# Kernel optimization log

Measured on AMD Instinct MI355X. Metric: run time of the kernel, lower is better.

Reference implementation:

```python
import jax, jax.numpy as jnp
import numpy as np

B, C, H, W = 16, 512, 32, 32
G = min(C // 4, 32)  # group-norm groups = 32
EPS = 1e-6


def setup_inputs() -> dict:
    key = jax.random.key(0)
    ks = jax.random.split(key, 9)
    s = 1.0 / np.sqrt(C)
    return {
        "x": jax.random.normal(ks[0], (B, C, H, W), dtype=jnp.float32),
        "gn_gamma": jnp.ones((C,), jnp.float32),
        "gn_beta": jnp.zeros((C,), jnp.float32),
        "W0": jax.random.normal(ks[1], (C, C), jnp.float32) * s,
        "b0": jnp.zeros((C,), jnp.float32),
        "W1": jax.random.normal(ks[2], (C, C), jnp.float32) * s,
        "b1": jnp.zeros((C,), jnp.float32),
        "W2": jax.random.normal(ks[3], (C, C), jnp.float32) * s,
        "b2": jnp.zeros((C,), jnp.float32),
        "W3": jax.random.normal(ks[4], (C, C), jnp.float32) * s,
        "b3": jnp.zeros((C,), jnp.float32),
    }


def _group_norm(x, gamma, beta):
    b, c, h, w = x.shape
    xg = x.reshape(b, G, c // G, h, w)
    mu = jnp.mean(xg, axis=(2, 3, 4), keepdims=True)
    var = jnp.var(xg, axis=(2, 3, 4), keepdims=True)
    xn = ((xg - mu) * jax.lax.rsqrt(var + EPS)).reshape(b, c, h, w)
    return xn * gamma[None, :, None, None] + beta[None, :, None, None]


def _nin(x, Wm, bv):
    # 1x1 conv via channel contraction: bchw,cd->bdhw
    return jnp.einsum('bchw,cd->bdhw', x, Wm) + bv[None, :, None, None]


def reference(x, gn_gamma, gn_beta, W0, b0, W1, b1, W2, b2, W3, b3):
    b, c, h, w = x.shape
    hn = _group_norm(x, gn_gamma, gn_beta)
    q = _nin(hn, W0, b0)
    k = _nin(hn, W1, b1)
    v = _nin(hn, W2, b2)
    # attention scores over all spatial positions: [b, h, w, i, j]
    scores = jnp.einsum('bchw,bcij->bhwij', q, k) * (c ** -0.5)
    attn = jax.nn.softmax(scores.reshape(b, h, w, h * w), axis=-1).reshape(b, h, w, h, w)
    o = jnp.einsum('bhwij,bcij->bchw', attn, v)
    o = _nin(o, W3, b3)
    return x + o  # skip_rescale=False
```

## Files before the change

kernel.cpp:

```cpp
#include <hip/hip_runtime.h>
#include <stdint.h>

typedef __bf16 bf16_t;
typedef _Float16 f16_t;
typedef bf16_t bf16x8 __attribute__((ext_vector_type(8)));
typedef bf16_t bf16x4 __attribute__((ext_vector_type(4)));
typedef f16_t  f16x8  __attribute__((ext_vector_type(8)));
typedef f16_t  f16x4  __attribute__((ext_vector_type(4)));
typedef float floatx4 __attribute__((ext_vector_type(4)));

static constexpr int NB  = 16;
static constexpr int NC  = 512;
static constexpr int NHW = 1024;
static constexpr int NG  = 32;
static constexpr int CPG = 16;

#define SCALE 0.044194173824159216f
#define LOG2E 1.4426950408889634f

__global__ __launch_bounds__(256) void gn_stats_k(const float* __restrict__ x,
                                                  float* __restrict__ stats) {
  int bg = blockIdx.x;
  const float* xp = x + (size_t)bg * CPG * NHW;
  float s = 0.f, ss = 0.f;
  for (int i = threadIdx.x * 4; i < CPG * NHW; i += 256 * 4) {
    float4 v = *(const float4*)&xp[i];
    s += v.x + v.y + v.z + v.w;
    ss += v.x * v.x + v.y * v.y + v.z * v.z + v.w * v.w;
  }
#pragma unroll
  for (int off = 1; off < 64; off <<= 1) {
    s  += __shfl_xor(s,  off, 64);
    ss += __shfl_xor(ss, off, 64);
  }
  __shared__ float red[2][4];
  int wv = threadIdx.x >> 6;
  if ((threadIdx.x & 63) == 0) { red[0][wv] = s; red[1][wv] = ss; }
  __syncthreads();
  if (threadIdx.x == 0) {
    float st  = red[0][0] + red[0][1] + red[0][2] + red[0][3];
    float sst = red[1][0] + red[1][1] + red[1][2] + red[1][3];
    float mean = st * (1.f / 16384.f);
    float var  = sst * (1.f / 16384.f) - mean * mean;
    stats[bg * 2]     = mean;
    stats[bg * 2 + 1] = rsqrtf(var + 1e-6f);
  }
}

__global__ __launch_bounds__(256) void gn_apply_k(const float* __restrict__ x,
                                                  const float* __restrict__ gamma,
                                                  const float* __restrict__ beta,
                                                  const float* __restrict__ stats,
                                                  bf16_t* __restrict__ hnT) {
  int bi = blockIdx.z;
  int c0 = blockIdx.y * 32;
  int n0 = blockIdx.x * 32;
  __shared__ float tile[32][33];
  int tn = threadIdx.x & 31;
  int tr = threadIdx.x >> 5;
  const float* xb = x + (size_t)bi * NC * NHW;
#pragma unroll
  for (int r = 0; r < 4; r++) {
    int c = c0 + tr + r * 8;
    int g = c >> 4;
    float mean = stats[(bi * NG + g) * 2];
    float rstd = stats[(bi * NG + g) * 2 + 1];
    float ga = gamma[c], be = beta[c];
    float v = xb[(size_t)c * NHW + n0 + tn];
    tile[tr + r * 8][tn] = (v - mean) * rstd * ga + be;
  }
  __syncthreads();
  bf16_t* hb = hnT + (size_t)bi * NHW * NC;
  int nl = threadIdx.x >> 3, cc = (threadIdx.x & 7) * 4;
  bf16x4 pk;
#pragma unroll
  for (int i = 0; i < 4; i++) pk[i] = (bf16_t)tile[cc + i][nl];
  *(bf16x4*)&hb[(size_t)(n0 + nl) * NC + c0 + cc] = pk;
}

__global__ __launch_bounds__(256) void wtrans_k(const float* __restrict__ W0,
                                                const float* __restrict__ W1,
                                                const float* __restrict__ W2,
                                                const float* __restrict__ W3,
                                                bf16_t* __restrict__ Wt) {
  int w = blockIdx.z;
  const float* W = (w == 0) ? W0 : (w == 1) ? W1 : (w == 2) ? W2 : W3;
  int d0 = blockIdx.x * 32, c0 = blockIdx.y * 32;
  __shared__ float tile[32][33];
  int tdx = threadIdx.x & 31, tr = threadIdx.x >> 5;
#pragma unroll
  for (int r = 0; r < 4; r++)
    tile[tr + r * 8][tdx] = W[(size_t)(c0 + tr + r * 8) * NC + d0 + tdx];
  __syncthreads();
  bf16_t* o = Wt + (size_t)w * NC * NC;
  int dl = threadIdx.x >> 3, cc = (threadIdx.x & 7) * 4;
  bf16x4 pk;
#pragma unroll
  for (int i = 0; i < 4; i++) pk[i] = (bf16_t)tile[cc + i][dl];
  *(bf16x4*)&o[(size_t)(d0 + dl) * NC + c0 + cc] = pk;
}

__device__ __forceinline__ void glds16(const bf16_t* g, bf16_t* lds) {
  __builtin_amdgcn_global_load_lds(
      (const __attribute__((address_space(1))) unsigned int*)g,
      (__attribute__((address_space(3))) unsigned int*)lds, 16, 0, 0);
}

__device__ __forceinline__ floatx4 mfma_bf16(bf16x8 a, bf16x8 b, floatx4 c) {
  return __builtin_amdgcn_mfma_f32_16x16x32_bf16(a, b, c, 0, 0, 0);
}

template<int KDIM, bool SWAP>
__device__ __forceinline__ void gemm_core(const bf16_t* __restrict__ A,
                                          const bf16_t* __restrict__ B,
                                          int m0, int n0,
                                          floatx4 (&acc)[4][4]) {
  __shared__ bf16_t As[128 * 64];
  __shared__ bf16_t Bs[128 * 64];
  const int tid = threadIdx.x, lane = tid & 63, wv = tid >> 6;
  const int l16 = lane & 15, quad = lane >> 4;
  const int wm = wv & 1, wn = wv >> 1;
  const int x7 = l16 & 7;

  const int srow = lane >> 3;
  const int schunk = (lane & 7) ^ srow;
  const bf16_t* aptr = A + (size_t)(m0 + wv * 32 + srow) * KDIM + schunk * 8;
  const bf16_t* bptr = B + (size_t)(n0 + wv * 32 + srow) * KDIM + schunk * 8;
  bf16_t* as_ = &As[(wv * 32) * 64];
  bf16_t* bs_ = &Bs[(wv * 32) * 64];

  for (int k0 = 0; k0 < KDIM; k0 += 64) {
    __syncthreads();
#pragma unroll
    for (int i = 0; i < 4; i++) {
      glds16(aptr + (size_t)(8 * i) * KDIM, as_ + (8 * i) * 64);
      glds16(bptr + (size_t)(8 * i) * KDIM, bs_ + (8 * i) * 64);
    }
    aptr += 64; bptr += 64;
    __syncthreads();
    bf16x8 af[2][4], bfv[2][4];
#pragma unroll
    for (int h = 0; h < 2; h++)
#pragma unroll
      for (int i = 0; i < 4; i++) {
        int q = h * 4 + quad;
        af[h][i]  = *(const bf16x8*)&As[(wm * 64 + i * 16 + l16) * 64 + ((q ^ x7) * 8)];
        bfv[h][i] = *(const bf16x8*)&Bs[(wn * 64 + i * 16 + l16) * 64 + ((q ^ x7) * 8)];
      }
#pragma unroll
    for (int h = 0; h < 2; h++)
#pragma unroll
      for (int i = 0; i < 4; i++)
#pragma unroll
        for (int j = 0; j < 4; j++)
          acc[i][j] = SWAP ? mfma_bf16(bfv[h][j], af[h][i], acc[i][j])
                           : mfma_bf16(af[h][i], bfv[h][j], acc[i][j]);
  }
}

#define ACC_INIT(acc)                                   \
  floatx4 acc[4][4];                                    \
  _Pragma("unroll") for (int i = 0; i < 4; i++)         \
  _Pragma("unroll") for (int j = 0; j < 4; j++)         \
    acc[i][j] = (floatx4){0.f, 0.f, 0.f, 0.f};

__global__ __launch_bounds__(256) void gemm_qk_k(const bf16_t* __restrict__ hnT,
                                                 const bf16_t* __restrict__ Wt,
                                                 const float* __restrict__ b0,
                                                 const float* __restrict__ b1,
                                                 bf16_t* __restrict__ Qt,
                                                 bf16_t* __restrict__ Kt) {
  int bz = blockIdx.z, bi = bz & 15, wsel = bz >> 4;
  int n0 = blockIdx.x * 128, m0 = blockIdx.y * 128;
  const bf16_t* A = hnT + (size_t)bi * NHW * NC;
  const bf16_t* B = Wt + (size_t)wsel * NC * NC;
  ACC_INIT(acc);
  gemm_core<NC, true>(A, B, m0, n0, acc);

  const int lane = threadIdx.x & 63, wv = threadIdx.x >> 6;
  const int l16 = lane & 15, quad = lane >> 4, wm = wv & 1, wn = wv >> 1;
  const float* bias = wsel ? b1 : b0;
  bf16_t* out = (wsel ? Kt : Qt) + (size_t)bi * NHW * NC;
#pragma unroll
  for (int i = 0; i < 4; i++) {
    int m = m0 + wm * 64 + i * 16 + l16;
#pragma unroll
    for (int j = 0; j < 4; j++) {
      int db = n0 + wn * 64 + j * 16 + quad * 4;
      float4 bv = *(const float4*)&bias[db];
      bf16x4 pk;
      pk[0] = (bf16_t)(acc[i][j][0] + bv.x);
      pk[1] = (bf16_t)(acc[i][j][1] + bv.y);
      pk[2] = (bf16_t)(acc[i][j][2] + bv.z);
      pk[3] = (bf16_t)(acc[i][j][3] + bv.w);
      *(bf16x4*)&out[(size_t)m * NC + db] = pk;
    }
  }
}

__global__ __launch_bounds__(256) void gemm_v_k(const bf16_t* __restrict__ hnT,
                                                const bf16_t* __restrict__ Wt2,
                                                const float* __restrict__ b2,
                                                bf16_t* __restrict__ Vm) {
  int bi = blockIdx.z;
  int n0 = blockIdx.x * 128, m0 = blockIdx.y * 128;
  const bf16_t* A = hnT + (size_t)bi * NHW * NC;
  ACC_INIT(acc);
  gemm_core<NC, false>(A, Wt2, m0, n0, acc);

  const int lane = threadIdx.x & 63, wv = threadIdx.x >> 6;
  const int l16 = lane & 15, quad = lane >> 4, wm = wv & 1, wn = wv >> 1;
  bf16_t* out = Vm + (size_t)bi * NC * NHW;
#pragma unroll
  for (int i = 0; i < 4; i++)
#pragma unroll
    for (int j = 0; j < 4; j++) {
      int row = m0 + wm * 64 + i * 16 + quad * 4;
      int col = n0 + wn * 64 + j * 16 + l16;
      float bv = b2[col];
      bf16x4 pk;
#pragma unroll
      for (int r = 0; r < 4; r++) pk[r] = (bf16_t)(acc[i][j][r] + bv);
      *(bf16x4*)&out[(size_t)col * NHW + row] = pk;
    }
}

__global__ __launch_bounds__(256) void gemm_s_k(const bf16_t* __restrict__ Qt,
                                                const bf16_t* __restrict__ Kt,
                                                f16_t* __restrict__ S) {
  int bi = blockIdx.z;
  int n0 = blockIdx.x * 128, m0 = blockIdx.y * 128;
  const bf16_t* A = Qt + (size_t)bi * NHW * NC;
  const bf16_t* B = Kt + (size_t)bi * NHW * NC;
  ACC_INIT(acc);
  gemm_core<NC, true>(A, B, m0, n0, acc);

  const int lane = threadIdx.x & 63, wv = threadIdx.x >> 6;
  const int l16 = lane & 15, quad = lane >> 4, wm = wv & 1, wn = wv >> 1;
  f16_t* out = S + (size_t)bi * NHW * NHW;
#pragma unroll
  for (int i = 0; i < 4; i++) {
    int m = m0 + wm * 64 + i * 16 + l16;
#pragma unroll
    for (int j = 0; j < 4; j++) {
      int nb = n0 + wn * 64 + j * 16 + quad * 4;
      f16x4 pk;
#pragma unroll
      for (int r = 0; r < 4; r++) pk[r] = (f16_t)(acc[i][j][r] * SCALE);
      *(f16x4*)&out[(size_t)m * NHW + nb] = pk;
    }
  }
}

__global__ __launch_bounds__(256) void softmax_k(const f16_t* __restrict__ S,
                                                 bf16_t* __restrict__ P) {
  int row = blockIdx.x * 4 + (threadIdx.x >> 6);
  int lane = threadIdx.x & 63;
  const f16_t* sp = S + (size_t)row * NHW + lane * 16;
  f16x8 a = *(const f16x8*)sp;
  f16x8 b = *(const f16x8*)(sp + 8);
  float v[16];
#pragma unroll
  for (int k = 0; k < 8; k++) { v[k] = (float)a[k]; v[8 + k] = (float)b[k]; }
  float mx = v[0];
#pragma unroll
  for (int k = 1; k < 16; k++) mx = fmaxf(mx, v[k]);
#pragma unroll
  for (int off = 1; off < 64; off <<= 1) mx = fmaxf(mx, __shfl_xor(mx, off, 64));
  float e[16], s = 0.f;
#pragma unroll
  for (int k = 0; k < 16; k++) { e[k] = exp2f((v[k] - mx) * LOG2E); s += e[k]; }
#pragma unroll
  for (int off = 1; off < 64; off <<= 1) s += __shfl_xor(s, off, 64);
  float inv = 1.f / s;
  bf16x8 o0, o1;
#pragma unroll
  for (int k = 0; k < 8; k++) { o0[k] = (bf16_t)(e[k] * inv); o1[k] = (bf16_t)(e[8 + k] * inv); }
  bf16_t* pp = P + (size_t)row * NHW + lane * 16;
  *(bf16x8*)pp = o0;
  *(bf16x8*)(pp + 8) = o1;
}

__global__ __launch_bounds__(256) void gemm_pv_k(const bf16_t* __restrict__ P,
                                                 const bf16_t* __restrict__ Vm,
                                                 bf16_t* __restrict__ Ot) {
  int bi = blockIdx.z;
  int n0 = blockIdx.x * 128, m0 = blockIdx.y * 128;
  const bf16_t* A = P + (size_t)bi * NHW * NHW;
  const bf16_t* B = Vm + (size_t)bi * NC * NHW;
  ACC_INIT(acc);
  gemm_core<NHW, true>(A, B, m0, n0, acc);

  const int lane = threadIdx.x & 63, wv = threadIdx.x >> 6;
  const int l16 = lane & 15, quad = lane >> 4, wm = wv & 1, wn = wv >> 1;
  bf16_t* out = Ot + (size_t)bi * NHW * NC;
#pragma unroll
  for (int i = 0; i < 4; i++) {
    int m = m0 + wm * 64 + i * 16 + l16;
#pragma unroll
    for (int j = 0; j < 4; j++) {
      int cb = n0 + wn * 64 + j * 16 + quad * 4;
      bf16x4 pk;
#pragma unroll
      for (int r = 0; r < 4; r++) pk[r] = (bf16_t)(acc[i][j][r]);
      *(bf16x4*)&out[(size_t)m * NC + cb] = pk;
    }
  }
}

__global__ __launch_bounds__(256) void gemm_fin_k(const bf16_t* __restrict__ Ot,
                                                  const bf16_t* __restrict__ W3t,
                                                  const float* __restrict__ b3,
                                                  const float* __restrict__ x,
                                                  float* __restrict__ outp) {
  int bi = blockIdx.z;
  int n0 = blockIdx.x * 128, m0 = blockIdx.y * 128;
  const bf16_t* A = Ot + (size_t)bi * NHW * NC;
  ACC_INIT(acc);
  gemm_core<NC, false>(A, W3t, m0, n0, acc);

  const int lane = threadIdx.x & 63, wv = threadIdx.x >> 6;
  const int l16 = lane & 15, quad = lane >> 4, wm = wv & 1, wn = wv >> 1;
  const float* xb = x + (size_t)bi * NC * NHW;
  float* ob = outp + (size_t)bi * NC * NHW;
#pragma unroll
  for (int i = 0; i < 4; i++)
#pragma unroll
    for (int j = 0; j < 4; j++) {
      int row = m0 + wm * 64 + i * 16 + quad * 4;
      int col = n0 + wn * 64 + j * 16 + l16;
      float bv = b3[col];
      size_t base = (size_t)col * NHW + row;
      float4 xv = *(const float4*)&xb[base];
      float4 pk;
      pk.x = acc[i][j][0] + bv + xv.x;
      pk.y = acc[i][j][1] + bv + xv.y;
      pk.z = acc[i][j][2] + bv + xv.z;
      pk.w = acc[i][j][3] + bv + xv.w;
      *(float4*)&ob[base] = pk;
    }
}

extern "C" void kernel_launch(void* const* d_in, const int* in_sizes, int n_in,
                              void* d_out, int out_size, void* d_ws, size_t ws_size,
                              hipStream_t stream) {
  (void)in_sizes; (void)n_in; (void)out_size; (void)ws_size;
  const float* x     = (const float*)d_in[0];
  const float* gamma = (const float*)d_in[1];
  const float* beta  = (const float*)d_in[2];
  const float* W0    = (const float*)d_in[3];
  const float* b0    = (const float*)d_in[4];
  const float* W1    = (const float*)d_in[5];
  const float* b1    = (const float*)d_in[6];
  const float* W2    = (const float*)d_in[7];
  const float* b2    = (const float*)d_in[8];
  const float* W3    = (const float*)d_in[9];
  const float* b3    = (const float*)d_in[10];
  float* outp = (float*)d_out;

  char* ws = (char*)d_ws;
  const size_t PLANE = (size_t)NB * NHW * NC * sizeof(bf16_t);
  float* stats = (float*)ws;
  size_t off = 4096;
  bf16_t* hnT = (bf16_t*)(ws + off); off += PLANE;
  bf16_t* Qt  = (bf16_t*)(ws + off); off += PLANE;
  bf16_t* Kt  = (bf16_t*)(ws + off); off += PLANE;
  bf16_t* Vm  = (bf16_t*)(ws + off); off += PLANE;
  bf16_t* Wt  = (bf16_t*)(ws + off); off += 4 * (size_t)NC * NC * sizeof(bf16_t);
  f16_t*  S   = (f16_t*)(ws + off);  off += (size_t)NB * NHW * NHW * sizeof(f16_t);
  bf16_t* P   = (bf16_t*)S;
  bf16_t* Ot  = hnT;

  gn_stats_k<<<NB * NG, 256, 0, stream>>>(x, stats);
  gn_apply_k<<<dim3(32, 16, NB), 256, 0, stream>>>(x, gamma, beta, stats, hnT);
  wtrans_k<<<dim3(16, 16, 4), 256, 0, stream>>>(W0, W1, W2, W3, Wt);
  gemm_qk_k<<<dim3(4, 8, 32), 256, 0, stream>>>(hnT, Wt, b0, b1, Qt, Kt);
  gemm_v_k<<<dim3(4, 8, NB), 256, 0, stream>>>(hnT, Wt + 2 * (size_t)NC * NC, b2, Vm);
  gemm_s_k<<<dim3(8, 8, NB), 256, 0, stream>>>(Qt, Kt, S);
  softmax_k<<<dim3(NB * NHW / 4), 256, 0, stream>>>(S, P);
  gemm_pv_k<<<dim3(4, 8, NB), 256, 0, stream>>>(P, Vm, Ot);
  gemm_fin_k<<<dim3(4, 8, NB), 256, 0, stream>>>(Ot, Wt + 3 * (size_t)NC * NC, b3, x, outp);
}
```

Measured before the change: 257.9 us.

## Fold V projection into output projection via precomputed W2·W3 product

Removes the per-batch V projection GEMM by using the associativity attn·(hn·W2)·W3 = (attn·hn)·(W2·W3): a small kernel computes the combined 512x512 weight once and a bias kernel folds b2·W3+b3, since softmax rows sum to one. GroupNorm apply now also writes a channel-major copy of hn to serve as the PV operand. The softmax scale moves from the score GEMM epilogue into the Q projection epilogue. This trades one large GEMM for a tiny weight GEMM, a serial bias loop and an extra hn write, and adds bf16 rounding of the combined weight.

```diff
diff --git a/kernel.cpp b/kernel.cpp
--- a/kernel.cpp
+++ b/kernel.cpp
@@ -51,7 +51,8 @@
                                                   const float* __restrict__ gamma,
                                                   const float* __restrict__ beta,
                                                   const float* __restrict__ stats,
-                                                  bf16_t* __restrict__ hnT) {
+                                                  bf16_t* __restrict__ hnT,
+                                                  bf16_t* __restrict__ hnN) {
   int bi = blockIdx.z;
   int c0 = blockIdx.y * 32;
   int n0 = blockIdx.x * 32;
@@ -70,12 +71,17 @@
     tile[tr + r * 8][tn] = (v - mean) * rstd * ga + be;
   }
   __syncthreads();
+  int rl = threadIdx.x >> 3, ch = (threadIdx.x & 7) * 4;
   bf16_t* hb = hnT + (size_t)bi * NHW * NC;
-  int nl = threadIdx.x >> 3, cc = (threadIdx.x & 7) * 4;
   bf16x4 pk;
 #pragma unroll
-  for (int i = 0; i < 4; i++) pk[i] = (bf16_t)tile[cc + i][nl];
-  *(bf16x4*)&hb[(size_t)(n0 + nl) * NC + c0 + cc] = pk;
+  for (int i = 0; i < 4; i++) pk[i] = (bf16_t)tile[ch + i][rl];
+  *(bf16x4*)&hb[(size_t)(n0 + rl) * NC + c0 + ch] = pk;
+  bf16_t* hc = hnN + (size_t)bi * NC * NHW;
+  bf16x4 pk2;
+#pragma unroll
+  for (int i = 0; i < 4; i++) pk2[i] = (bf16_t)tile[rl][ch + i];
+  *(bf16x4*)&hc[(size_t)(c0 + rl) * NHW + n0 + ch] = pk2;
 }
 
 __global__ __launch_bounds__(256) void wtrans_k(const float* __restrict__ W0,
@@ -85,19 +91,37 @@
                                                 bf16_t* __restrict__ Wt) {
   int w = blockIdx.z;
   const float* W = (w == 0) ? W0 : (w == 1) ? W1 : (w == 2) ? W2 : W3;
+  bf16_t* o = Wt + (size_t)w * NC * NC;
   int d0 = blockIdx.x * 32, c0 = blockIdx.y * 32;
+  if (w == 2) {
+    int cl = threadIdx.x >> 3, dc = (threadIdx.x & 7) * 4;
+    float4 v = *(const float4*)&W[(size_t)(c0 + cl) * NC + d0 + dc];
+    bf16x4 pk;
+    pk[0] = (bf16_t)v.x; pk[1] = (bf16_t)v.y; pk[2] = (bf16_t)v.z; pk[3] = (bf16_t)v.w;
+    *(bf16x4*)&o[(size_t)(c0 + cl) * NC + d0 + dc] = pk;
+    return;
+  }
   __shared__ float tile[32][33];
   int tdx = threadIdx.x & 31, tr = threadIdx.x >> 5;
 #pragma unroll
   for (int r = 0; r < 4; r++)
     tile[tr + r * 8][tdx] = W[(size_t)(c0 + tr + r * 8) * NC + d0 + tdx];
   __syncthreads();
-  bf16_t* o = Wt + (size_t)w * NC * NC;
   int dl = threadIdx.x >> 3, cc = (threadIdx.x & 7) * 4;
   bf16x4 pk;
 #pragma unroll
   for (int i = 0; i < 4; i++) pk[i] = (bf16_t)tile[cc + i][dl];
   *(bf16x4*)&o[(size_t)(d0 + dl) * NC + c0 + cc] = pk;
+}
+
+__global__ __launch_bounds__(256) void bias_k(const float* __restrict__ b2,
+                                              const float* __restrict__ W3,
+                                              const float* __restrict__ b3,
+                                              float* __restrict__ bb) {
+  int e = blockIdx.x * 256 + threadIdx.x;
+  float s = b3[e];
+  for (int d = 0; d < NC; d++) s += b2[d] * W3[(size_t)d * NC + e];
+  bb[e] = s;
 }
 
 __device__ __forceinline__ void glds16(const bf16_t* g, bf16_t* lds) {
@@ -163,6 +187,26 @@
   _Pragma("unroll") for (int i = 0; i < 4; i++)         \
   _Pragma("unroll") for (int j = 0; j < 4; j++)         \
     acc[i][j] = (floatx4){0.f, 0.f, 0.f, 0.f};
+
+__global__ __launch_bounds__(256) void w23_k(const bf16_t* __restrict__ Wt3,
+                                             const bf16_t* __restrict__ W2b,
+                                             bf16_t* __restrict__ W23t) {
+  int n0 = blockIdx.x * 128, m0 = blockIdx.y * 128;
+  ACC_INIT(acc);
+  gemm_core<NC, false>(Wt3, W2b, m0, n0, acc);
+  const int lane = threadIdx.x & 63, wv = threadIdx.x >> 6;
+  const int l16 = lane & 15, quad = lane >> 4, wm = wv & 1, wn = wv >> 1;
+#pragma unroll
+  for (int i = 0; i < 4; i++)
+#pragma unroll
+    for (int j = 0; j < 4; j++) {
+      int row = m0 + wm * 64 + i * 16 + quad * 4;
+      int col = n0 + wn * 64 + j * 16 + l16;
+#pragma unroll
+      for (int r = 0; r < 4; r++)
+        W23t[(size_t)(row + r) * NC + col] = (bf16_t)acc[i][j][r];
+    }
+}
 
 __global__ __launch_bounds__(256) void gemm_qk_k(const bf16_t* __restrict__ hnT,
                                                  const bf16_t* __restrict__ Wt,
@@ -180,6 +224,7 @@
   const int lane = threadIdx.x & 63, wv = threadIdx.x >> 6;
   const int l16 = lane & 15, quad = lane >> 4, wm = wv & 1, wn = wv >> 1;
   const float* bias = wsel ? b1 : b0;
+  const float sc = wsel ? 1.f : SCALE;
   bf16_t* out = (wsel ? Kt : Qt) + (size_t)bi * NHW * NC;
 #pragma unroll
   for (int i = 0; i < 4; i++) {
@@ -189,40 +234,13 @@
       int db = n0 + wn * 64 + j * 16 + quad * 4;
       float4 bv = *(const float4*)&bias[db];
       bf16x4 pk;
-      pk[0] = (bf16_t)(acc[i][j][0] + bv.x);
-      pk[1] = (bf16_t)(acc[i][j][1] + bv.y);
-      pk[2] = (bf16_t)(acc[i][j][2] + bv.z);
-      pk[3] = (bf16_t)(acc[i][j][3] + bv.w);
+      pk[0] = (bf16_t)((acc[i][j][0] + bv.x) * sc);
+      pk[1] = (bf16_t)((acc[i][j][1] + bv.y) * sc);
+      pk[2] = (bf16_t)((acc[i][j][2] + bv.z) * sc);
+      pk[3] = (bf16_t)((acc[i][j][3] + bv.w) * sc);
       *(bf16x4*)&out[(size_t)m * NC + db] = pk;
     }
   }
-}
-
-__global__ __launch_bounds__(256) void gemm_v_k(const bf16_t* __restrict__ hnT,
-                                                const bf16_t* __restrict__ Wt2,
-                                                const float* __restrict__ b2,
-                                                bf16_t* __restrict__ Vm) {
-  int bi = blockIdx.z;
-  int n0 = blockIdx.x * 128, m0 = blockIdx.y * 128;
-  const bf16_t* A = hnT + (size_t)bi * NHW * NC;
-  ACC_INIT(acc);
-  gemm_core<NC, false>(A, Wt2, m0, n0, acc);
-
-  const int lane = threadIdx.x & 63, wv = threadIdx.x >> 6;
-  const int l16 = lane & 15, quad = lane >> 4, wm = wv & 1, wn = wv >> 1;
-  bf16_t* out = Vm + (size_t)bi * NC * NHW;
-#pragma unroll
-  for (int i = 0; i < 4; i++)
-#pragma unroll
-    for (int j = 0; j < 4; j++) {
-      int row = m0 + wm * 64 + i * 16 + quad * 4;
-      int col = n0 + wn * 64 + j * 16 + l16;
-      float bv = b2[col];
-      bf16x4 pk;
-#pragma unroll
-      for (int r = 0; r < 4; r++) pk[r] = (bf16_t)(acc[i][j][r] + bv);
-      *(bf16x4*)&out[(size_t)col * NHW + row] = pk;
-    }
 }
 
 __global__ __launch_bounds__(256) void gemm_s_k(const bf16_t* __restrict__ Qt,
@@ -246,7 +264,7 @@
       int nb = n0 + wn * 64 + j * 16 + quad * 4;
       f16x4 pk;
 #pragma unroll
-      for (int r = 0; r < 4; r++) pk[r] = (f16_t)(acc[i][j][r] * SCALE);
+      for (int r = 0; r < 4; r++) pk[r] = (f16_t)(acc[i][j][r]);
       *(f16x4*)&out[(size_t)m * NHW + nb] = pk;
     }
   }
@@ -281,19 +299,19 @@
   *(bf16x8*)(pp + 8) = o1;
 }
 
-__global__ __launch_bounds__(256) void gemm_pv_k(const bf16_t* __restrict__ P,
-                                                 const bf16_t* __restrict__ Vm,
-                                                 bf16_t* __restrict__ Ot) {
+__global__ __launch_bounds__(256) void gemm_t_k(const bf16_t* __restrict__ P,
+                                                const bf16_t* __restrict__ hnN,
+                                                bf16_t* __restrict__ T) {
   int bi = blockIdx.z;
   int n0 = blockIdx.x * 128, m0 = blockIdx.y * 128;
   const bf16_t* A = P + (size_t)bi * NHW * NHW;
-  const bf16_t* B = Vm + (size_t)bi * NC * NHW;
+  const bf16_t* B = hnN + (size_t)bi * NC * NHW;
   ACC_INIT(acc);
   gemm_core<NHW, true>(A, B, m0, n0, acc);
 
   const int lane = threadIdx.x & 63, wv = threadIdx.x >> 6;
   const int l16 = lane & 15, quad = lane >> 4, wm = wv & 1, wn = wv >> 1;
-  bf16_t* out = Ot + (size_t)bi * NHW * NC;
+  bf16_t* out = T + (size_t)bi * NHW * NC;
 #pragma unroll
   for (int i = 0; i < 4; i++) {
     int m = m0 + wm * 64 + i * 16 + l16;
@@ -308,16 +326,16 @@
   }
 }
 
-__global__ __launch_bounds__(256) void gemm_fin_k(const bf16_t* __restrict__ Ot,
-                                                  const bf16_t* __restrict__ W3t,
-                                                  const float* __restrict__ b3,
+__global__ __launch_bounds__(256) void gemm_out_k(const bf16_t* __restrict__ T,
+                                                  const bf16_t* __restrict__ W23t,
+                                                  const float* __restrict__ bb,
                                                   const float* __restrict__ x,
                                                   float* __restrict__ outp) {
   int bi = blockIdx.z;
   int n0 = blockIdx.x * 128, m0 = blockIdx.y * 128;
-  const bf16_t* A = Ot + (size_t)bi * NHW * NC;
+  const bf16_t* A = T + (size_t)bi * NHW * NC;
   ACC_INIT(acc);
-  gemm_core<NC, false>(A, W3t, m0, n0, acc);
+  gemm_core<NC, false>(A, W23t, m0, n0, acc);
 
   const int lane = threadIdx.x & 63, wv = threadIdx.x >> 6;
   const int l16 = lane & 15, quad = lane >> 4, wm = wv & 1, wn = wv >> 1;
@@ -329,7 +347,7 @@
     for (int j = 0; j < 4; j++) {
       int row = m0 + wm * 64 + i * 16 + quad * 4;
       int col = n0 + wn * 64 + j * 16 + l16;
-      float bv = b3[col];
+      float bv = bb[col];
       size_t base = (size_t)col * NHW + row;
       float4 xv = *(const float4*)&xb[base];
       float4 pk;
@@ -363,21 +381,24 @@
   float* stats = (float*)ws;
   size_t off = 4096;
   bf16_t* hnT = (bf16_t*)(ws + off); off += PLANE;
+  bf16_t* hnN = (bf16_t*)(ws + off); off += PLANE;
   bf16_t* Qt  = (bf16_t*)(ws + off); off += PLANE;
   bf16_t* Kt  = (bf16_t*)(ws + off); off += PLANE;
-  bf16_t* Vm  = (bf16_t*)(ws + off); off += PLANE;
   bf16_t* Wt  = (bf16_t*)(ws + off); off += 4 * (size_t)NC * NC * sizeof(bf16_t);
+  bf16_t* W23t = (bf16_t*)(ws + off); off += (size_t)NC * NC * sizeof(bf16_t);
+  float*  bb  = (float*)(ws + off);  off += 4096;
   f16_t*  S   = (f16_t*)(ws + off);  off += (size_t)NB * NHW * NHW * sizeof(f16_t);
   bf16_t* P   = (bf16_t*)S;
-  bf16_t* Ot  = hnT;
+  bf16_t* T   = hnT;
 
   gn_stats_k<<<NB * NG, 256, 0, stream>>>(x, stats);
-  gn_apply_k<<<dim3(32, 16, NB), 256, 0, stream>>>(x, gamma, beta, stats, hnT);
+  gn_apply_k<<<dim3(32, 16, NB), 256, 0, stream>>>(x, gamma, beta, stats, hnT, hnN);
   wtrans_k<<<dim3(16, 16, 4), 256, 0, stream>>>(W0, W1, W2, W3, Wt);
+  w23_k<<<dim3(4, 4, 1), 256, 0, stream>>>(Wt + 3 * (size_t)NC * NC, Wt + 2 * (size_t)NC * NC, W23t);
+  bias_k<<<dim3(2), 256, 0, stream>>>(b2, W3, b3, bb);
   gemm_qk_k<<<dim3(4, 8, 32), 256, 0, stream>>>(hnT, Wt, b0, b1, Qt, Kt);
-  gemm_v_k<<<dim3(4, 8, NB), 256, 0, stream>>>(hnT, Wt + 2 * (size_t)NC * NC, b2, Vm);
   gemm_s_k<<<dim3(8, 8, NB), 256, 0, stream>>>(Qt, Kt, S);
   softmax_k<<<dim3(NB * NHW / 4), 256, 0, stream>>>(S, P);
-  gemm_pv_k<<<dim3(4, 8, NB), 256, 0, stream>>>(P, Vm, Ot);
-  gemm_fin_k<<<dim3(4, 8, NB), 256, 0, stream>>>(Ot, Wt + 3 * (size_t)NC * NC, b3, x, outp);
-}
+  gemm_t_k<<<dim3(4, 8, NB), 256, 0, stream>>>(P, hnN, T);
+  gemm_out_k<<<dim3(4, 8, NB), 256, 0, stream>>>(T, W23t, bb, x, outp);
+}
```

Result: slower. 268.0 us (+3.9%).
